# Performance work log

Measured on AMD Instinct MI355X. Metric: run time of the kernel, lower is better.

## Reference

```python
import jax, jax.numpy as jnp
import numpy as np

ZERO_THRESH = 1e-20
N_ECC, N_POLAR = 15, 20          # 300 log-polar pooling windows
MIN_ECC, MAX_ECC = 0.5, 15.0      # degrees
NUM_SCALES, N_ORI = 4, 4          # order=3 -> 4 orientations
BASE_RES = 512


def _make_windows(res):
    """Mostly-zero log-polar Gaussian pooling windows, (N_ECC*N_POLAR, res, res)."""
    ys, xs = np.meshgrid(np.arange(res) - res / 2 + 0.5,
                         np.arange(res) - res / 2 + 0.5, indexing='ij')
    deg_per_pix = MAX_ECC / (res / 2)
    r = np.sqrt(xs ** 2 + ys ** 2) * deg_per_pix
    logr = np.log(np.maximum(r, 1e-6))
    theta = np.arctan2(ys, xs)
    mus_e = np.linspace(np.log(MIN_ECC), np.log(MAX_ECC), N_ECC)
    se = mus_e[1] - mus_e[0]
    mus_a = np.linspace(-np.pi, np.pi, N_POLAR, endpoint=False)
    sa = 2 * np.pi / N_POLAR
    dth = ((theta[None] - mus_a[:, None, None] + np.pi) % (2 * np.pi)) - np.pi
    ang = np.exp(-0.5 * (dth / sa) ** 2)                              # (P,H,W)
    rad = np.exp(-0.5 * ((logr[None] - mus_e[:, None, None]) / se) ** 2)  # (E,H,W)
    w = (rad[:, None] * ang[None]).reshape(N_ECC * N_POLAR, res, res)
    w[w < 1e-6] = 0.0   # enforce the sparse (mostly-zero) structure
    return w.astype(np.float32)


def setup_inputs() -> dict:
    key = jax.random.key(0)
    ks = jax.random.split(key, 6)
    inp = {'image': jax.random.uniform(ks[0], (BASE_RES, BASE_RES), dtype=jnp.float32)}
    for s in range(NUM_SCALES):
        res = BASE_RES >> s
        # complex pyramid coefficients: (orientations, H_s, W_s, [real, imag])
        inp[f'pyr{s}'] = jax.random.normal(ks[1 + s], (N_ORI, res, res, 2), dtype=jnp.float32)
        inp[f'win{s}'] = jnp.asarray(_make_windows(res))
    return inp


def reference(image, pyr0, pyr1, pyr2, pyr3, win0, win1, win2, win3):
    img = image[None, None]                       # (1,1,H,W) as in forward's unsqueeze
    parts = []
    for p, w in zip((pyr0, pyr1, pyr2, pyr3), (win0, win1, win2, win3)):
        # complex modulus: sqrt(re^2 + im^2), (O, H_s, W_s)
        m = jnp.sqrt(jnp.sum(p * p, axis=-1))
        # number of non-zero pixels per window
        wnp = jnp.sum(w > ZERO_THRESH, axis=(-1, -2)).astype(m.dtype)   # (W,)
        # windowed sum fused (einsum ijkl,wkl->ijwkl then sum(-1,-2) == direct contraction)
        pooled = jnp.einsum('okl,wkl->ow', m, w) / wnp
        parts.append(pooled.reshape(-1))          # orientation-major, matches dict order
    wnp0 = jnp.sum(win0 > ZERO_THRESH, axis=(-1, -2)).astype(img.dtype)
    mean_lum = (jnp.einsum('ijkl,wkl->ijw', img, win0) / wnp0).reshape(-1)
    return jnp.concatenate(parts + [mean_lum])
```

## Files before the change

### kernel.cpp

```cpp
#include <hip/hip_runtime.h>
#include <math.h>


#define THREADS 256
#define T32F 27.631021f
#define BAND 2e-3f
#define TLO (T32F - BAND)
#define THI (T32F + BAND)
#define INV_SE 4.1161880f
#define INV_SA 3.1830989f

#define D_LNHALF -0.6931471805599453
#define D_LN15    2.7080502011022101
#define D_SE     ((D_LN15 - D_LNHALF) / 14.0)
#define D_SA     (6.283185307179586 / 20.0)
#define D_PI      3.141592653589793
#define D_2PI     6.283185307179586

#define A2_S0 8192
#define A4_S0 532480
#define A2_S1 1581056
#define A4_S1 1712128
#define A2_S2 1974272
#define A4_S2 2007040
#define A2_S3 2072576
#define A4_S3 2080768

__device__ __forceinline__ void build_px(const float* __restrict__ pyr,
                                         float* __restrict__ ws,
                                         int a2off, int a4off,
                                         int px, int res, int lg)
{
    int HW = res * res;
    int i = px >> lg, j = px & (res - 1);
    float cc = (float)res * 0.5f - 0.5f;
    float ys = (float)i - cc, xs = (float)j - cc;
    float r  = sqrtf(xs * xs + ys * ys) * (30.f / (float)res);
    float lr = logf(fmaxf(r, 1e-6f));
    float pc = (atan2f(ys, xs) + 3.14159265f) * INV_SA;
    *(float2*)(ws + a2off + 2 * (size_t)px) = make_float2(pc, lr);
    float4 m;
    float2 c0 = *(const float2*)(pyr + 2 * ((size_t)0 * HW + px));
    float2 c1 = *(const float2*)(pyr + 2 * ((size_t)1 * HW + px));
    float2 c2 = *(const float2*)(pyr + 2 * ((size_t)2 * HW + px));
    float2 c3 = *(const float2*)(pyr + 2 * ((size_t)3 * HW + px));
    m.x = sqrtf(fmaf(c0.x, c0.x, c0.y * c0.y));
    m.y = sqrtf(fmaf(c1.x, c1.x, c1.y * c1.y));
    m.z = sqrtf(fmaf(c2.x, c2.x, c2.y * c2.y));
    m.w = sqrtf(fmaf(c3.x, c3.x, c3.y * c3.y));
    *(float4*)(ws + a4off + 4 * (size_t)px) = m;
}

__global__ __launch_bounds__(THREADS)
void build_tables(const float* __restrict__ pyr0, const float* __restrict__ pyr1,
                  const float* __restrict__ pyr2, const float* __restrict__ pyr3,
                  float* __restrict__ ws)
{
    int bid = blockIdx.x, tid = threadIdx.x;
    if (bid < 1024)      build_px(pyr0, ws, A2_S0, A4_S0, (bid << 8) | tid,          512, 9);
    else if (bid < 1280) build_px(pyr1, ws, A2_S1, A4_S1, ((bid - 1024) << 8) | tid, 256, 8);
    else if (bid < 1344) build_px(pyr2, ws, A2_S2, A4_S2, ((bid - 1280) << 8) | tid, 128, 7);
    else                 build_px(pyr3, ws, A2_S3, A4_S3, ((bid - 1344) << 8) | tid,  64, 6);
}

template <bool HAS_IMG>
__device__ __forceinline__ void pool_tile(const float* __restrict__ A2,
                                          const float* __restrict__ A4,
                                          const float* __restrict__ img,
                                          float* __restrict__ ws,
                                          int res, int lg, double dppd,
                                          int scale, int x0, int y0, int triple)
{
    float cc  = (float)res * 0.5f - 0.5f;
    float xlo = (float)x0 - cc, xhi = xlo + 31.f;
    float ylo = (float)y0 - cc, yhi = ylo + 31.f;
    float dx = fmaxf(fmaxf(xlo, -xhi), 0.f);
    float dy = fmaxf(fmaxf(ylo, -yhi), 0.f);
    float dppf = 30.f / (float)res;
    float rmin = sqrtf(dx * dx + dy * dy) * dppf;
    float rmax = sqrtf(fmaxf(xlo * xlo, xhi * xhi) + fmaxf(ylo * ylo, yhi * yhi)) * dppf;
    float lrmin = logf(fmaxf(rmin, 1e-6f));
    float lrmax = logf(fmaxf(rmax, 1e-6f));
    float mue_lo = (float)(3 * triple) * 0.24294267f - 0.69314718f;
    float mue_hi = (float)(3 * triple + 2) * 0.24294267f - 0.69314718f;
    if (lrmin > mue_hi + 1.2790f || lrmax < mue_lo - 1.2790f) return;

    const int tid = threadIdx.x, lane = tid & 63, wave = tid >> 6;
    const int l_p = lane % 20;
    const int e   = 3 * triple + lane / 20;
    const bool lane_ok = (lane < 60);
    const double mue_d = (e == 14) ? D_LN15 : ((double)e * D_SE + D_LNHALF);
    const double mua_d = (double)l_p * D_SA - D_PI;
    const float Aq = lane_ok ? (float)(mue_d / D_SE) : 1e18f;
    const float pf = (float)l_p;

    float v0 = 0.f, v1 = 0.f, v2 = 0.f, v3 = 0.f, vc = 0.f, vi = 0.f;

#pragma unroll 4
    for (int k = 0; k < 256; ++k) {
        int t = wave * 256 + k;
        int i = y0 + (t >> 5);
        int j = x0 + (t & 31);
        int px = __builtin_amdgcn_readfirstlane((i << lg) + j);
        float2 t2 = *(const float2*)(A2 + 2 * (size_t)px);
        float4 t4 = *(const float4*)(A4 + 4 * (size_t)px);
        float gi = HAS_IMG ? img[px] : 0.f;

        float qa = t2.x - pf;
        qa = (qa > 10.f) ? qa - 20.f : qa;
        qa = (qa < -10.f) ? qa + 20.f : qa;
        float qr = fmaf(t2.y, INV_SE, -Aq);
        float s  = fmaf(qa, qa, qr * qr);
        float wv = (s <= TLO) ? __expf(-0.5f * s) : 0.f;
        float al = (s <= TLO) ? 1.f : 0.f;
        if (__ballot(s > TLO && s <= THI)) {
            if (s > TLO && s <= THI) {
                double ys = (double)i - (double)res * 0.5 + 0.5;
                double xs = (double)j - (double)res * 0.5 + 0.5;
                double rd  = sqrt(xs * xs + ys * ys) * dppd;
                double lrd = log(fmax(rd, 1e-6));
                double thd = atan2(ys, xs);
                double dd  = thd - mua_d + D_PI;
                double md  = fmod(dd, D_2PI);
                if (md < 0.0) md += D_2PI;
                double ta = (md - D_PI) / D_SA;
                double tr = (lrd - mue_d) / D_SE;
                double w64 = exp(-0.5 * tr * tr) * exp(-0.5 * ta * ta);
                bool alive = (w64 >= 1e-6);
                wv = alive ? (float)w64 : 0.f;
                al = alive ? 1.f : 0.f;
            }
        }
        v0 = fmaf(wv, t4.x, v0);
        v1 = fmaf(wv, t4.y, v1);
        v2 = fmaf(wv, t4.z, v2);
        v3 = fmaf(wv, t4.w, v3);
        vc += al;
        if (HAS_IMG) vi = fmaf(wv, gi, vi);
    }

    __shared__ float facc[4][360];
    if (lane_ok) {
        float* f = &facc[wave][lane * 6];
        f[0] = v0; f[1] = v1; f[2] = v2; f[3] = v3; f[4] = vc; f[5] = vi;
    }
    __syncthreads();
    for (int idx = tid; idx < 360; idx += THREADS) {
        float v = facc[0][idx] + facc[1][idx] + facc[2][idx] + facc[3][idx];
        if (v == 0.f) continue;
        int l = idx / 6, f = idx - l * 6;
        int w = (3 * triple + l / 20) * 20 + (l % 20);
        if (f < 4)       atomicAdd(&ws[scale * 1200 + f * 300 + w], v);
        else if (f == 4) atomicAdd(&ws[4800 + scale * 300 + w], v);
        else if (HAS_IMG) atomicAdd(&ws[6000 + w], v);
    }
}

__global__ __launch_bounds__(THREADS)
void pool_kernel(const float* __restrict__ image, float* __restrict__ ws)
{
    int bid = blockIdx.x;
    if (bid < 1280) {
        int triple = bid % 5, tile = bid / 5;
        pool_tile<true>(ws + A2_S0, ws + A4_S0, image, ws, 512, 9, 15.0 / 256.0,
                        0, (tile & 15) * 32, (tile >> 4) * 32, triple);
    } else if (bid < 1600) {
        int l = bid - 1280, triple = l % 5, tile = l / 5;
        pool_tile<false>(ws + A2_S1, ws + A4_S1, nullptr, ws, 256, 8, 15.0 / 128.0,
                         1, (tile & 7) * 32, (tile >> 3) * 32, triple);
    } else if (bid < 1680) {
        int l = bid - 1600, triple = l % 5, tile = l / 5;
        pool_tile<false>(ws + A2_S2, ws + A4_S2, nullptr, ws, 128, 7, 15.0 / 64.0,
                         2, (tile & 3) * 32, (tile >> 2) * 32, triple);
    } else {
        int l = bid - 1680, triple = l % 5, tile = l / 5;
        pool_tile<false>(ws + A2_S3, ws + A4_S3, nullptr, ws, 64, 6, 15.0 / 32.0,
                         3, (tile & 1) * 32, (tile >> 1) * 32, triple);
    }
}

__global__ __launch_bounds__(THREADS)
void finalize_kernel(const float* __restrict__ ws, float* __restrict__ out)
{
    int i = blockIdx.x * blockDim.x + threadIdx.x;
    if (i >= 5100) return;
    float v;
    if (i < 4800) {
        int s = i / 1200;
        int w = i % 300;
        v = ws[i] / ws[4800 + s * 300 + w];
    } else {
        int w = i - 4800;
        v = ws[6000 + w] / ws[4800 + w];
    }
    out[i] = v;
}

extern "C" void kernel_launch(void* const* d_in, const int* in_sizes, int n_in,
                              void* d_out, int out_size, void* d_ws, size_t ws_size,
                              hipStream_t stream)
{
    const float* image = (const float*)d_in[0];
    const float* pyr0  = (const float*)d_in[1];
    const float* pyr1  = (const float*)d_in[3];
    const float* pyr2  = (const float*)d_in[5];
    const float* pyr3  = (const float*)d_in[7];
    float* ws  = (float*)d_ws;
    float* out = (float*)d_out;

    hipMemsetAsync(d_ws, 0, 6300 * sizeof(float), stream);
    build_tables<<<1360, THREADS, 0, stream>>>(pyr0, pyr1, pyr2, pyr3, ws);
    pool_kernel<<<1700, THREADS, 0, stream>>>(image, ws);
    finalize_kernel<<<20, THREADS, 0, stream>>>(ws, out);
}
```

Before: 555.8 us.

## Interleave per-pixel tables, stage tiles in LDS, defer border recomputation to fixup kernel

```diff
diff --git a/kernel.cpp b/kernel.cpp
--- a/kernel.cpp
+++ b/kernel.cpp
@@ -7,7 +7,7 @@
 #define BAND 2e-3f
 #define TLO (T32F - BAND)
 #define THI (T32F + BAND)
-#define INV_SE 4.1161880f
+#define INV_SE 4.1161881f
 #define INV_SA 3.1830989f
 
 #define D_LNHALF -0.6931471805599453
@@ -17,19 +17,17 @@
 #define D_PI      3.141592653589793
 #define D_2PI     6.283185307179586
 
-#define A2_S0 8192
-#define A4_S0 532480
-#define A2_S1 1581056
-#define A4_S1 1712128
-#define A2_S2 1974272
-#define A4_S2 2007040
-#define A2_S3 2072576
-#define A4_S3 2080768
+#define T8_S0 8192
+#define T8_S1 (T8_S0 + 262144 * 8)
+#define T8_S2 (T8_S1 + 65536 * 8)
+#define T8_S3 (T8_S2 + 16384 * 8)
+#define LIST_OFF 3000000
+#define LIST_CAP 1000000
 
 __device__ __forceinline__ void build_px(const float* __restrict__ pyr,
+                                         const float* __restrict__ img,
                                          float* __restrict__ ws,
-                                         int a2off, int a4off,
-                                         int px, int res, int lg)
+                                         int t8off, int px, int res, int lg)
 {
     int HW = res * res;
     int i = px >> lg, j = px & (res - 1);
@@ -38,37 +36,39 @@
     float r  = sqrtf(xs * xs + ys * ys) * (30.f / (float)res);
     float lr = logf(fmaxf(r, 1e-6f));
     float pc = (atan2f(ys, xs) + 3.14159265f) * INV_SA;
-    *(float2*)(ws + a2off + 2 * (size_t)px) = make_float2(pc, lr);
-    float4 m;
     float2 c0 = *(const float2*)(pyr + 2 * ((size_t)0 * HW + px));
     float2 c1 = *(const float2*)(pyr + 2 * ((size_t)1 * HW + px));
     float2 c2 = *(const float2*)(pyr + 2 * ((size_t)2 * HW + px));
     float2 c3 = *(const float2*)(pyr + 2 * ((size_t)3 * HW + px));
-    m.x = sqrtf(fmaf(c0.x, c0.x, c0.y * c0.y));
-    m.y = sqrtf(fmaf(c1.x, c1.x, c1.y * c1.y));
-    m.z = sqrtf(fmaf(c2.x, c2.x, c2.y * c2.y));
-    m.w = sqrtf(fmaf(c3.x, c3.x, c3.y * c3.y));
-    *(float4*)(ws + a4off + 4 * (size_t)px) = m;
-}
-
-__global__ __launch_bounds__(THREADS)
-void build_tables(const float* __restrict__ pyr0, const float* __restrict__ pyr1,
+    float4 A, B;
+    A.x = pc; A.y = lr;
+    A.z = sqrtf(fmaf(c0.x, c0.x, c0.y * c0.y));
+    A.w = sqrtf(fmaf(c1.x, c1.x, c1.y * c1.y));
+    B.x = sqrtf(fmaf(c2.x, c2.x, c2.y * c2.y));
+    B.y = sqrtf(fmaf(c3.x, c3.x, c3.y * c3.y));
+    B.z = img ? img[px] : 0.f;
+    B.w = 0.f;
+    *(float4*)(ws + t8off + (size_t)px * 8)     = A;
+    *(float4*)(ws + t8off + (size_t)px * 8 + 4) = B;
+}
+
+__global__ __launch_bounds__(THREADS)
+void build_tables(const float* __restrict__ image,
+                  const float* __restrict__ pyr0, const float* __restrict__ pyr1,
                   const float* __restrict__ pyr2, const float* __restrict__ pyr3,
                   float* __restrict__ ws)
 {
     int bid = blockIdx.x, tid = threadIdx.x;
-    if (bid < 1024)      build_px(pyr0, ws, A2_S0, A4_S0, (bid << 8) | tid,          512, 9);
-    else if (bid < 1280) build_px(pyr1, ws, A2_S1, A4_S1, ((bid - 1024) << 8) | tid, 256, 8);
-    else if (bid < 1344) build_px(pyr2, ws, A2_S2, A4_S2, ((bid - 1280) << 8) | tid, 128, 7);
-    else                 build_px(pyr3, ws, A2_S3, A4_S3, ((bid - 1344) << 8) | tid,  64, 6);
+    if (bid < 1024)      build_px(pyr0, image,   ws, T8_S0, (bid << 8) | tid,          512, 9);
+    else if (bid < 1280) build_px(pyr1, nullptr, ws, T8_S1, ((bid - 1024) << 8) | tid, 256, 8);
+    else if (bid < 1344) build_px(pyr2, nullptr, ws, T8_S2, ((bid - 1280) << 8) | tid, 128, 7);
+    else                 build_px(pyr3, nullptr, ws, T8_S3, ((bid - 1344) << 8) | tid,  64, 6);
 }
 
 template <bool HAS_IMG>
-__device__ __forceinline__ void pool_tile(const float* __restrict__ A2,
-                                          const float* __restrict__ A4,
-                                          const float* __restrict__ img,
+__device__ __forceinline__ void pool_tile(const float* __restrict__ tbl8,
                                           float* __restrict__ ws,
-                                          int res, int lg, double dppd,
+                                          int res, int lg,
                                           int scale, int x0, int y0, int triple)
 {
     float cc  = (float)res * 0.5f - 0.5f;
@@ -86,11 +86,26 @@
     if (lrmin > mue_hi + 1.2790f || lrmax < mue_lo - 1.2790f) return;
 
     const int tid = threadIdx.x, lane = tid & 63, wave = tid >> 6;
+
+    __shared__ float sh[4][2048];
+    __shared__ float facc[4][360];
+    float* my = sh[wave];
+    {
+        int j = x0 + (lane >> 1);
+        int half = (lane & 1) * 4;
+#pragma unroll
+        for (int r = 0; r < 8; ++r) {
+            int i = y0 + wave * 8 + r;
+            float4 v = *(const float4*)(tbl8 + ((size_t)((i << lg) + j)) * 8 + half);
+            *(float4*)(my + r * 256 + lane * 4) = v;
+        }
+    }
+    __syncthreads();
+
     const int l_p = lane % 20;
     const int e   = 3 * triple + lane / 20;
     const bool lane_ok = (lane < 60);
     const double mue_d = (e == 14) ? D_LN15 : ((double)e * D_SE + D_LNHALF);
-    const double mua_d = (double)l_p * D_SA - D_PI;
     const float Aq = lane_ok ? (float)(mue_d / D_SE) : 1e18f;
     const float pf = (float)l_p;
 
@@ -98,48 +113,35 @@
 
 #pragma unroll 4
     for (int k = 0; k < 256; ++k) {
-        int t = wave * 256 + k;
-        int i = y0 + (t >> 5);
-        int j = x0 + (t & 31);
-        int px = __builtin_amdgcn_readfirstlane((i << lg) + j);
-        float2 t2 = *(const float2*)(A2 + 2 * (size_t)px);
-        float4 t4 = *(const float4*)(A4 + 4 * (size_t)px);
-        float gi = HAS_IMG ? img[px] : 0.f;
-
-        float qa = t2.x - pf;
+        float4 A = *(const float4*)(my + k * 8);
+        float4 B = *(const float4*)(my + k * 8 + 4);
+        float qa = A.x - pf;
         qa = (qa > 10.f) ? qa - 20.f : qa;
         qa = (qa < -10.f) ? qa + 20.f : qa;
-        float qr = fmaf(t2.y, INV_SE, -Aq);
+        float qr = fmaf(A.y, INV_SE, -Aq);
         float s  = fmaf(qa, qa, qr * qr);
-        float wv = (s <= TLO) ? __expf(-0.5f * s) : 0.f;
-        float al = (s <= TLO) ? 1.f : 0.f;
-        if (__ballot(s > TLO && s <= THI)) {
-            if (s > TLO && s <= THI) {
-                double ys = (double)i - (double)res * 0.5 + 0.5;
-                double xs = (double)j - (double)res * 0.5 + 0.5;
-                double rd  = sqrt(xs * xs + ys * ys) * dppd;
-                double lrd = log(fmax(rd, 1e-6));
-                double thd = atan2(ys, xs);
-                double dd  = thd - mua_d + D_PI;
-                double md  = fmod(dd, D_2PI);
-                if (md < 0.0) md += D_2PI;
-                double ta = (md - D_PI) / D_SA;
-                double tr = (lrd - mue_d) / D_SE;
-                double w64 = exp(-0.5 * tr * tr) * exp(-0.5 * ta * ta);
-                bool alive = (w64 >= 1e-6);
-                wv = alive ? (float)w64 : 0.f;
-                al = alive ? 1.f : 0.f;
+        bool alive = (s <= TLO);
+        float wv = alive ? __expf(-0.5f * s) : 0.f;
+        v0 = fmaf(wv, A.z, v0);
+        v1 = fmaf(wv, A.w, v1);
+        v2 = fmaf(wv, B.x, v2);
+        v3 = fmaf(wv, B.y, v3);
+        vc += alive ? 1.f : 0.f;
+        if (HAS_IMG) vi = fmaf(wv, B.z, vi);
+        bool bord = (s > TLO) & (s <= THI);
+        if (__builtin_expect(__ballot(bord) != 0ull, 0)) {
+            if (bord & lane_ok) {
+                int row = wave * 8 + (k >> 5);
+                int px  = ((y0 + row) << lg) + x0 + (k & 31);
+                unsigned idx = atomicAdd((unsigned*)(ws + 6300), 1u);
+                if (idx < LIST_CAP)
+                    ((unsigned*)(ws + LIST_OFF))[idx] =
+                        (unsigned)px | ((unsigned)l_p << 18) |
+                        ((unsigned)e << 23) | ((unsigned)scale << 27);
             }
         }
-        v0 = fmaf(wv, t4.x, v0);
-        v1 = fmaf(wv, t4.y, v1);
-        v2 = fmaf(wv, t4.z, v2);
-        v3 = fmaf(wv, t4.w, v3);
-        vc += al;
-        if (HAS_IMG) vi = fmaf(wv, gi, vi);
-    }
-
-    __shared__ float facc[4][360];
+    }
+
     if (lane_ok) {
         float* f = &facc[wave][lane * 6];
         f[0] = v0; f[1] = v1; f[2] = v2; f[3] = v3; f[4] = vc; f[5] = vi;
@@ -150,32 +152,73 @@
         if (v == 0.f) continue;
         int l = idx / 6, f = idx - l * 6;
         int w = (3 * triple + l / 20) * 20 + (l % 20);
-        if (f < 4)       atomicAdd(&ws[scale * 1200 + f * 300 + w], v);
-        else if (f == 4) atomicAdd(&ws[4800 + scale * 300 + w], v);
+        if (f < 4)        atomicAdd(&ws[scale * 1200 + f * 300 + w], v);
+        else if (f == 4)  atomicAdd(&ws[4800 + scale * 300 + w], v);
         else if (HAS_IMG) atomicAdd(&ws[6000 + w], v);
     }
 }
 
 __global__ __launch_bounds__(THREADS)
-void pool_kernel(const float* __restrict__ image, float* __restrict__ ws)
+void pool_kernel(float* __restrict__ ws)
 {
     int bid = blockIdx.x;
     if (bid < 1280) {
         int triple = bid % 5, tile = bid / 5;
-        pool_tile<true>(ws + A2_S0, ws + A4_S0, image, ws, 512, 9, 15.0 / 256.0,
-                        0, (tile & 15) * 32, (tile >> 4) * 32, triple);
+        pool_tile<true>(ws + T8_S0, ws, 512, 9, 0, (tile & 15) * 32, (tile >> 4) * 32, triple);
     } else if (bid < 1600) {
         int l = bid - 1280, triple = l % 5, tile = l / 5;
-        pool_tile<false>(ws + A2_S1, ws + A4_S1, nullptr, ws, 256, 8, 15.0 / 128.0,
-                         1, (tile & 7) * 32, (tile >> 3) * 32, triple);
+        pool_tile<false>(ws + T8_S1, ws, 256, 8, 1, (tile & 7) * 32, (tile >> 3) * 32, triple);
     } else if (bid < 1680) {
         int l = bid - 1600, triple = l % 5, tile = l / 5;
-        pool_tile<false>(ws + A2_S2, ws + A4_S2, nullptr, ws, 128, 7, 15.0 / 64.0,
-                         2, (tile & 3) * 32, (tile >> 2) * 32, triple);
+        pool_tile<false>(ws + T8_S2, ws, 128, 7, 2, (tile & 3) * 32, (tile >> 2) * 32, triple);
     } else {
         int l = bid - 1680, triple = l % 5, tile = l / 5;
-        pool_tile<false>(ws + A2_S3, ws + A4_S3, nullptr, ws, 64, 6, 15.0 / 32.0,
-                         3, (tile & 1) * 32, (tile >> 1) * 32, triple);
+        pool_tile<false>(ws + T8_S3, ws, 64, 6, 3, (tile & 1) * 32, (tile >> 1) * 32, triple);
+    }
+}
+
+__global__ __launch_bounds__(THREADS)
+void fixup_kernel(float* __restrict__ ws)
+{
+    unsigned n = ((unsigned*)(ws))[6300];
+    if (n > LIST_CAP) n = LIST_CAP;
+    for (unsigned idx = blockIdx.x * blockDim.x + threadIdx.x; idx < n;
+         idx += gridDim.x * blockDim.x) {
+        unsigned rec = ((const unsigned*)(ws + LIST_OFF))[idx];
+        int px    = rec & 0x3FFFF;
+        int p     = (rec >> 18) & 31;
+        int e     = (rec >> 23) & 15;
+        int scale = (rec >> 27) & 3;
+        int res, lg, t8; double dpp;
+        if (scale == 0)      { res = 512; lg = 9; t8 = T8_S0; dpp = 15.0 / 256.0; }
+        else if (scale == 1) { res = 256; lg = 8; t8 = T8_S1; dpp = 15.0 / 128.0; }
+        else if (scale == 2) { res = 128; lg = 7; t8 = T8_S2; dpp = 15.0 / 64.0; }
+        else                 { res = 64;  lg = 6; t8 = T8_S3; dpp = 15.0 / 32.0; }
+        int i = px >> lg, j = px & (res - 1);
+        double ys = (double)i - (double)res * 0.5 + 0.5;
+        double xs = (double)j - (double)res * 0.5 + 0.5;
+        double rd  = sqrt(xs * xs + ys * ys) * dpp;
+        double lrd = log(fmax(rd, 1e-6));
+        double thd = atan2(ys, xs);
+        double mue = (e == 14) ? D_LN15 : ((double)e * D_SE + D_LNHALF);
+        double mua = (double)p * D_SA - D_PI;
+        double dd  = thd - mua + D_PI;
+        double md  = fmod(dd, D_2PI);
+        if (md < 0.0) md += D_2PI;
+        double ta = (md - D_PI) / D_SA;
+        double tr = (lrd - mue) / D_SE;
+        double w64 = exp(-0.5 * tr * tr) * exp(-0.5 * ta * ta);
+        if (w64 >= 1e-6) {
+            float wv = (float)w64;
+            const float* pxd = ws + t8 + (size_t)px * 8;
+            int w = e * 20 + p;
+            atomicAdd(&ws[scale * 1200 + 0 * 300 + w], wv * pxd[2]);
+            atomicAdd(&ws[scale * 1200 + 1 * 300 + w], wv * pxd[3]);
+            atomicAdd(&ws[scale * 1200 + 2 * 300 + w], wv * pxd[4]);
+            atomicAdd(&ws[scale * 1200 + 3 * 300 + w], wv * pxd[5]);
+            atomicAdd(&ws[4800 + scale * 300 + w], 1.f);
+            if (scale == 0) atomicAdd(&ws[6000 + w], wv * pxd[6]);
+        }
     }
 }
 
@@ -208,8 +251,9 @@
     float* ws  = (float*)d_ws;
     float* out = (float*)d_out;
 
-    hipMemsetAsync(d_ws, 0, 6300 * sizeof(float), stream);
-    build_tables<<<1360, THREADS, 0, stream>>>(pyr0, pyr1, pyr2, pyr3, ws);
-    pool_kernel<<<1700, THREADS, 0, stream>>>(image, ws);
+    hipMemsetAsync(d_ws, 0, 6304 * sizeof(float), stream);
+    build_tables<<<1360, THREADS, 0, stream>>>(image, pyr0, pyr1, pyr2, pyr3, ws);
+    pool_kernel<<<1700, THREADS, 0, stream>>>(ws);
+    fixup_kernel<<<8, THREADS, 0, stream>>>(ws);
     finalize_kernel<<<20, THREADS, 0, stream>>>(ws, out);
 }
```

Result: faster. 494.0 us (-11.1%).
